# Kernel optimization log

Hardware: AMD Instinct MI355X
Metric: run time of the kernel (lower is better)

## Reference

```python
import jax, jax.numpy as jnp
import numpy as np

TOL = 1e-4
MAX_ITER = 50
D = 512
B = 16384

def setup_inputs() -> dict:
    key = jax.random.key(0)
    kx, kw = jax.random.split(key)
    x = jax.random.normal(kx, (B, D), dtype=jnp.float32)
    # nn.Linear default init: U(-1/sqrt(d), 1/sqrt(d)), bias=False
    bound = 1.0 / np.sqrt(D)
    W = jax.random.uniform(kw, (D, D), dtype=jnp.float32, minval=-bound, maxval=bound)
    return {"x": x, "W": W}

def reference(x, W):
    # Fixed-point iteration z <- tanh(z @ W^T + x).
    # Torch uses a data-dependent while loop with early break; here we run a
    # fixed-length scan and freeze z once the convergence criterion fires,
    # which reproduces the same converged value (z is held constant after
    # ||z_next - z|| < tol, exactly like breaking out of the loop).
    z0 = jnp.zeros_like(x)

    def step(carry, _):
        z, done = carry
        z_next = jnp.tanh(z @ W.T + x)          # [B, D]
        err = jnp.linalg.norm(z_next - z)        # global Frobenius norm, like torch.norm
        z_new = jnp.where(done, z, z_next)       # freeze after convergence (early-exit)
        done = done | (err < TOL)
        return (z_new, done), None

    (z, _), _ = jax.lax.scan(step, (z0, jnp.array(False)), None, length=MAX_ITER)
    return z
```

## Files before the change

kernel.cpp:

```cpp
#include <hip/hip_runtime.h>


typedef short s8v  __attribute__((ext_vector_type(8)));
typedef float f32x16 __attribute__((ext_vector_type(16)));

#define BATCH 16384
#define DIM   512
#define TM    64
#define NITER 50

__device__ __forceinline__ unsigned short f2bf(float f) {
    unsigned int u = __float_as_uint(f);
    u += 0x7fffu + ((u >> 16) & 1u);
    return (unsigned short)(u >> 16);
}

__device__ __forceinline__ float fast_tanh(float v) {
    v = fminf(10.0f, fmaxf(-10.0f, v));
    float t = __builtin_amdgcn_exp2f(v * 2.8853900817779268f);
    return (t - 1.0f) * __builtin_amdgcn_rcpf(t + 1.0f);
}

__device__ __forceinline__ f32x16 zero16() {
    f32x16 v;
#pragma unroll
    for (int i = 0; i < 16; ++i) v[i] = 0.0f;
    return v;
}

__global__ void wprep_kernel(const float* __restrict__ W, unsigned short* __restrict__ Wf) {
    int tid = blockIdx.x * blockDim.x + threadIdx.x;
    int jt  = tid >> 11;
    int rem = tid & 2047;
    int ks  = rem >> 6;
    int L   = rem & 63;
    int j   = jt * 32 + (L & 31);
    int k   = ks * 16 + (L >> 5) * 8;
    const float* src = W + j * DIM + k;
    uint4 p;
    p.x = (unsigned)f2bf(src[0]) | ((unsigned)f2bf(src[1]) << 16);
    p.y = (unsigned)f2bf(src[2]) | ((unsigned)f2bf(src[3]) << 16);
    p.z = (unsigned)f2bf(src[4]) | ((unsigned)f2bf(src[5]) << 16);
    p.w = (unsigned)f2bf(src[6]) | ((unsigned)f2bf(src[7]) << 16);
    ((uint4*)Wf)[tid] = p;
}

__device__ __forceinline__ int z_addr(int r, int j) {
    int c  = j >> 3;
    int lo = j & 7;
    return r * DIM + (((c ^ (r & 7)) << 3) | lo);
}

__global__ __launch_bounds__(512, 2)
void fixpoint_kernel(const float* __restrict__ x,
                     const unsigned short* __restrict__ Wf,
                     float* __restrict__ out) {
    __shared__ alignas(16) unsigned short zt[TM * DIM];

    const int tid  = threadIdx.x;
    const int lane = tid & 63;
    const int w    = tid >> 6;
    const int l31  = lane & 31;
    const int h    = lane >> 5;
    const int r0   = blockIdx.x * TM;
    const int jt0  = 2 * w;

    for (int idx = tid; idx < TM * DIM; idx += 512) {
        int r = idx >> 9, j = idx & (DIM - 1);
        zt[z_addr(r, j)] = f2bf(fast_tanh(x[(size_t)(r0 + r) * DIM + j]));
    }
    __syncthreads();

    const s8v* Wfv = (const s8v*)Wf;
    const int swz = l31 & 7;

    for (int it = 0; it < NITER - 1; ++it) {
        f32x16 acc00 = zero16(), acc01 = zero16(), acc10 = zero16(), acc11 = zero16();

#pragma unroll 4
        for (int ks = 0; ks < 32; ++ks) {
            s8v a0 = Wfv[(jt0 * 32 + ks) * 64 + lane];
            s8v a1 = Wfv[((jt0 + 1) * 32 + ks) * 64 + lane];
            int c = ((2 * ks + h) ^ swz) << 3;
            s8v b0 = *(const s8v*)&zt[l31 * DIM + c];
            s8v b1 = *(const s8v*)&zt[(l31 + 32) * DIM + c];
            acc00 = __builtin_amdgcn_mfma_f32_32x32x16_bf16(a0, b0, acc00, 0, 0, 0);
            acc01 = __builtin_amdgcn_mfma_f32_32x32x16_bf16(a0, b1, acc01, 0, 0, 0);
            acc10 = __builtin_amdgcn_mfma_f32_32x32x16_bf16(a1, b0, acc10, 0, 0, 0);
            acc11 = __builtin_amdgcn_mfma_f32_32x32x16_bf16(a1, b1, acc11, 0, 0, 0);
        }
        __syncthreads();

        const bool last = (it == NITER - 2);

        auto epi = [&](const f32x16& acc, int jb, int rl) {
            const size_t rowoff = (size_t)(r0 + rl) * DIM;
#pragma unroll
            for (int g = 0; g < 4; ++g) {
                int j0 = jb + 8 * g + 4 * h;
                const float4 xv = *(const float4*)&x[rowoff + j0];
                float v0 = fast_tanh(acc[4 * g + 0] + xv.x);
                float v1 = fast_tanh(acc[4 * g + 1] + xv.y);
                float v2 = fast_tanh(acc[4 * g + 2] + xv.z);
                float v3 = fast_tanh(acc[4 * g + 3] + xv.w);
                uint2 p;
                p.x = (unsigned)f2bf(v0) | ((unsigned)f2bf(v1) << 16);
                p.y = (unsigned)f2bf(v2) | ((unsigned)f2bf(v3) << 16);
                *(uint2*)&zt[z_addr(rl, j0)] = p;
                if (last) {
                    float4 o; o.x = v0; o.y = v1; o.z = v2; o.w = v3;
                    *(float4*)&out[rowoff + j0] = o;
                }
            }
        };
        epi(acc00, w * 64,      l31);
        epi(acc01, w * 64,      l31 + 32);
        epi(acc10, w * 64 + 32, l31);
        epi(acc11, w * 64 + 32, l31 + 32);
        __syncthreads();
    }
}

extern "C" void kernel_launch(void* const* d_in, const int* in_sizes, int n_in,
                              void* d_out, int out_size, void* d_ws, size_t ws_size,
                              hipStream_t stream) {
    const float* x = (const float*)d_in[0];
    const float* W = (const float*)d_in[1];
    float* out = (float*)d_out;
    unsigned short* Wf = (unsigned short*)d_ws;

    wprep_kernel<<<128, 256, 0, stream>>>(W, Wf);
    fixpoint_kernel<<<BATCH / TM, 512, 0, stream>>>(x, Wf, out);
}
```

Baseline: 580.5 us.

## Double-buffer z in LDS, keep scaled x in registers, cheaper tanh

Result: slower. 1.181 ms (+103.4%).

```diff
diff --git a/kernel.cpp b/kernel.cpp
--- a/kernel.cpp
+++ b/kernel.cpp
@@ -1,13 +1,14 @@
 #include <hip/hip_runtime.h>
 
 
-typedef short s8v  __attribute__((ext_vector_type(8)));
+typedef short s8v   __attribute__((ext_vector_type(8)));
 typedef float f32x16 __attribute__((ext_vector_type(16)));
 
 #define BATCH 16384
 #define DIM   512
 #define TM    64
 #define NITER 50
+#define L2E2  2.8853900817779268f
 
 __device__ __forceinline__ unsigned short f2bf(float f) {
     unsigned int u = __float_as_uint(f);
@@ -15,10 +16,10 @@
     return (unsigned short)(u >> 16);
 }
 
-__device__ __forceinline__ float fast_tanh(float v) {
-    v = fminf(10.0f, fmaxf(-10.0f, v));
-    float t = __builtin_amdgcn_exp2f(v * 2.8853900817779268f);
-    return (t - 1.0f) * __builtin_amdgcn_rcpf(t + 1.0f);
+__device__ __forceinline__ float tanh_e(float arg) {
+    float t = __builtin_amdgcn_exp2f(arg);
+    float r = __builtin_amdgcn_rcpf(t + 1.0f);
+    return fmaf(-2.0f, r, 1.0f);
 }
 
 __device__ __forceinline__ f32x16 zero16() {
@@ -45,17 +46,11 @@
     ((uint4*)Wf)[tid] = p;
 }
 
-__device__ __forceinline__ int z_addr(int r, int j) {
-    int c  = j >> 3;
-    int lo = j & 7;
-    return r * DIM + (((c ^ (r & 7)) << 3) | lo);
-}
-
 __global__ __launch_bounds__(512, 2)
 void fixpoint_kernel(const float* __restrict__ x,
                      const unsigned short* __restrict__ Wf,
                      float* __restrict__ out) {
-    __shared__ alignas(16) unsigned short zt[TM * DIM];
+    extern __shared__ unsigned short zb[];
 
     const int tid  = threadIdx.x;
     const int lane = tid & 63;
@@ -63,60 +58,84 @@
     const int l31  = lane & 31;
     const int h    = lane >> 5;
     const int r0   = blockIdx.x * TM;
-    const int jt0  = 2 * w;
 
-    for (int idx = tid; idx < TM * DIM; idx += 512) {
-        int r = idx >> 9, j = idx & (DIM - 1);
-        zt[z_addr(r, j)] = f2bf(fast_tanh(x[(size_t)(r0 + r) * DIM + j]));
+    float4 xr[2][8];
+#pragma unroll
+    for (int rt = 0; rt < 2; ++rt) {
+        const float* xrow = x + (size_t)(r0 + rt * 32 + l31) * DIM;
+#pragma unroll
+        for (int t = 0; t < 8; ++t) {
+            int j0 = w * 64 + (t >> 2) * 32 + (t & 3) * 8 + 4 * h;
+            float4 v = *(const float4*)&xrow[j0];
+            v.x *= L2E2; v.y *= L2E2; v.z *= L2E2; v.w *= L2E2;
+            xr[rt][t] = v;
+        }
     }
+
+#pragma unroll
+    for (int rt = 0; rt < 2; ++rt)
+#pragma unroll
+        for (int t = 0; t < 8; ++t) {
+            int j0 = w * 64 + (t >> 2) * 32 + (t & 3) * 8 + 4 * h;
+            float4 a = xr[rt][t];
+            float v0 = tanh_e(a.x), v1 = tanh_e(a.y);
+            float v2 = tanh_e(a.z), v3 = tanh_e(a.w);
+            uint2 p;
+            p.x = ((unsigned)f2bf(v1) << 16) | f2bf(v0);
+            p.y = ((unsigned)f2bf(v3) << 16) | f2bf(v2);
+            int e = ((rt * 32 + (j0 >> 4)) * 64 + ((j0 >> 3) & 1) * 32 + l31) * 8 + (j0 & 7);
+            *(uint2*)&zb[e] = p;
+        }
     __syncthreads();
 
-    const s8v* Wfv = (const s8v*)Wf;
-    const int swz = l31 & 7;
+    const s8v* Wv = (const s8v*)Wf + w * 4096 + lane;
 
     for (int it = 0; it < NITER - 1; ++it) {
+        const s8v* zcv = (const s8v*)(zb + (it & 1) * 32768) + lane;
+        unsigned short* zn = zb + ((it + 1) & 1) * 32768;
+
         f32x16 acc00 = zero16(), acc01 = zero16(), acc10 = zero16(), acc11 = zero16();
 
-#pragma unroll 4
+#pragma unroll
         for (int ks = 0; ks < 32; ++ks) {
-            s8v a0 = Wfv[(jt0 * 32 + ks) * 64 + lane];
-            s8v a1 = Wfv[((jt0 + 1) * 32 + ks) * 64 + lane];
-            int c = ((2 * ks + h) ^ swz) << 3;
-            s8v b0 = *(const s8v*)&zt[l31 * DIM + c];
-            s8v b1 = *(const s8v*)&zt[(l31 + 32) * DIM + c];
+            s8v a0 = Wv[ks * 64];
+            s8v a1 = Wv[ks * 64 + 2048];
+            s8v b0 = zcv[ks * 64];
+            s8v b1 = zcv[ks * 64 + 2048];
             acc00 = __builtin_amdgcn_mfma_f32_32x32x16_bf16(a0, b0, acc00, 0, 0, 0);
             acc01 = __builtin_amdgcn_mfma_f32_32x32x16_bf16(a0, b1, acc01, 0, 0, 0);
             acc10 = __builtin_amdgcn_mfma_f32_32x32x16_bf16(a1, b0, acc10, 0, 0, 0);
             acc11 = __builtin_amdgcn_mfma_f32_32x32x16_bf16(a1, b1, acc11, 0, 0, 0);
         }
-        __syncthreads();
 
         const bool last = (it == NITER - 2);
 
-        auto epi = [&](const f32x16& acc, int jb, int rl) {
-            const size_t rowoff = (size_t)(r0 + rl) * DIM;
+        auto epi = [&](const f32x16& acc, int tb, int rt) {
 #pragma unroll
             for (int g = 0; g < 4; ++g) {
-                int j0 = jb + 8 * g + 4 * h;
-                const float4 xv = *(const float4*)&x[rowoff + j0];
-                float v0 = fast_tanh(acc[4 * g + 0] + xv.x);
-                float v1 = fast_tanh(acc[4 * g + 1] + xv.y);
-                float v2 = fast_tanh(acc[4 * g + 2] + xv.z);
-                float v3 = fast_tanh(acc[4 * g + 3] + xv.w);
+                int t  = tb + g;
+                int j0 = w * 64 + tb * 8 + g * 8 + 4 * h;
+                float4 a = xr[rt][t];
+                float v0 = tanh_e(fmaf(acc[4 * g + 0], L2E2, a.x));
+                float v1 = tanh_e(fmaf(acc[4 * g + 1], L2E2, a.y));
+                float v2 = tanh_e(fmaf(acc[4 * g + 2], L2E2, a.z));
+                float v3 = tanh_e(fmaf(acc[4 * g + 3], L2E2, a.w));
                 uint2 p;
-                p.x = (unsigned)f2bf(v0) | ((unsigned)f2bf(v1) << 16);
-                p.y = (unsigned)f2bf(v2) | ((unsigned)f2bf(v3) << 16);
-                *(uint2*)&zt[z_addr(rl, j0)] = p;
+                p.x = ((unsigned)f2bf(v1) << 16) | f2bf(v0);
+                p.y = ((unsigned)f2bf(v3) << 16) | f2bf(v2);
+                int e = ((rt * 32 + (j0 >> 4)) * 64 + ((j0 >> 3) & 1) * 32 + l31) * 8 + (j0 & 7);
+                *(uint2*)&zn[e] = p;
                 if (last) {
                     float4 o; o.x = v0; o.y = v1; o.z = v2; o.w = v3;
-                    *(float4*)&out[rowoff + j0] = o;
+                    *(float4*)&out[(size_t)(r0 + rt * 32 + l31) * DIM + j0] = o;
                 }
             }
         };
-        epi(acc00, w * 64,      l31);
-        epi(acc01, w * 64,      l31 + 32);
-        epi(acc10, w * 64 + 32, l31);
-        epi(acc11, w * 64 + 32, l31 + 32);
+        epi(acc00, 0, 0);
+        epi(acc10, 4, 0);
+        epi(acc01, 0, 1);
+        epi(acc11, 4, 1);
+
         __syncthreads();
     }
 }
@@ -129,6 +148,8 @@
     float* out = (float*)d_out;
     unsigned short* Wf = (unsigned short*)d_ws;
 
+    hipFuncSetAttribute((const void*)fixpoint_kernel,
+                        hipFuncAttributeMaxDynamicSharedMemorySize, 131072);
     wprep_kernel<<<128, 256, 0, stream>>>(W, Wf);
-    fixpoint_kernel<<<BATCH / TM, 512, 0, stream>>>(x, Wf, out);
+    fixpoint_kernel<<<BATCH / TM, 512, 131072, stream>>>(x, Wf, out);
 }
```
